# Optimization experiments

Hardware: AMD Instinct MI355X
Metric: run time of the kernel (lower is better)

## Reference

```python
import jax, jax.numpy as jnp
import numpy as np

STRIDE = 2
P = 2


def setup_inputs() -> dict:
    key = jax.random.key(0)
    x = jax.random.normal(key, (32, 256, 64, 64), dtype=jnp.float32)
    return {"x": x}


def reference(x) -> jnp.ndarray:
    s = STRIDE
    b, c, h, w = x.shape
    # circular pad on the right/bottom if spatial dims are odd
    pad_h = h % 2
    pad_w = w % 2
    if pad_h or pad_w:
        x = jnp.pad(x, ((0, 0), (0, 0), (0, pad_h), (0, pad_w)), mode="wrap")
    h2, w2 = x.shape[2] // s, x.shape[3] // s
    # all s*s polyphase components: comps[i*s+j] == x[:, :, i::s, j::s]
    comps = x.reshape(b, c, h2, s, w2, s)
    comps = comps.transpose(3, 5, 0, 1, 2, 4).reshape(s * s, b, c, h2, w2)
    # p-norm per (component, batch) over channels + spatial dims
    norms = jnp.sum(jnp.abs(comps) ** P, axis=(2, 3, 4)) ** (1.0 / P)  # [s*s, b]
    max_idx = jnp.argmax(norms, axis=0)  # [b]
    selected = comps[max_idx, jnp.arange(b)]  # [b, c, h2, w2]
    return selected
```

## Files before the change

kernel.cpp:

```cpp
#include <hip/hip_runtime.h>


#define B 32
#define C 256
#define H 64
#define W 64
#define H2 32
#define W2 32
#define NBLK 64
#define IN_F4_PER_BATCH (C * H * W / 4)
#define PAIRS_PER_BATCH (IN_F4_PER_BATCH / 2)
#define OUT_F4_PER_BATCH (C * H2 * W2 / 4)

typedef float floatx4 __attribute__((ext_vector_type(4)));

__global__ __launch_bounds__(256) void aps_partials(const float4* __restrict__ x,
                                                    float* __restrict__ ws) {
    const int b = blockIdx.y;
    const float4* xb = x + (size_t)b * IN_F4_PER_BATCH;
    float s0 = 0.f, s1 = 0.f, s2 = 0.f, s3 = 0.f;
    for (int g = blockIdx.x * blockDim.x + threadIdx.x; g < PAIRS_PER_BATCH;
         g += gridDim.x * blockDim.x) {
        const int base = ((g >> 4) << 5) + (g & 15);
        float4 ve = xb[base];
        float4 vo = xb[base + 16];
        s0 += ve.x * ve.x + ve.z * ve.z;
        s1 += ve.y * ve.y + ve.w * ve.w;
        s2 += vo.x * vo.x + vo.z * vo.z;
        s3 += vo.y * vo.y + vo.w * vo.w;
    }
    for (int off = 32; off; off >>= 1) {
        s0 += __shfl_down(s0, off);
        s1 += __shfl_down(s1, off);
        s2 += __shfl_down(s2, off);
        s3 += __shfl_down(s3, off);
    }
    __shared__ float sm[4][4];
    const int lane = threadIdx.x & 63;
    const int wave = threadIdx.x >> 6;
    if (lane == 0) {
        sm[wave][0] = s0; sm[wave][1] = s1; sm[wave][2] = s2; sm[wave][3] = s3;
    }
    __syncthreads();
    if (threadIdx.x < 4) {
        const int k = threadIdx.x;
        float t = sm[0][k] + sm[1][k] + sm[2][k] + sm[3][k];
        ws[(b * 4 + k) * NBLK + blockIdx.x] = t;
    }
}

__global__ __launch_bounds__(256) void aps_gather(const float* __restrict__ x,
                                                  const float* __restrict__ ws,
                                                  float* __restrict__ out) {
    const int b = blockIdx.y;
    const int lane = threadIdx.x & 63;
    const int wave = threadIdx.x >> 6;
    float p = ws[(b * 4 + wave) * NBLK + lane];
    for (int off = 32; off; off >>= 1) p += __shfl_down(p, off);
    __shared__ float s4[4];
    if (lane == 0) s4[wave] = p;
    __syncthreads();
    float v0 = s4[0], v1 = s4[1], v2 = s4[2], v3 = s4[3];
    float best = v0;
    int k = 0;
    if (v1 > best) { best = v1; k = 1; }
    if (v2 > best) { best = v2; k = 2; }
    if (v3 > best) { k = 3; }
    const int di = k >> 1;
    const int dj = k & 1;

    const int idx = blockIdx.x * blockDim.x + threadIdx.x;
    const int t4 = idx & 7;
    const int i  = (idx >> 3) & 31;
    const int c  = idx >> 8;
    const float* row = x + (((size_t)(b * C + c) * H) + (2 * i + di)) * W;
    const float4* r4 = (const float4*)row + 2 * t4;
    float4 a  = r4[0];
    float4 bb = r4[1];
    floatx4 o;
    if (dj == 0) { o.x = a.x; o.y = a.z; o.z = bb.x; o.w = bb.z; }
    else         { o.x = a.y; o.y = a.w; o.z = bb.y; o.w = bb.w; }
    floatx4* op = (floatx4*)(out + ((size_t)b * OUT_F4_PER_BATCH + idx) * 4);
    __builtin_nontemporal_store(o, op);
}

extern "C" void kernel_launch(void* const* d_in, const int* in_sizes, int n_in,
                              void* d_out, int out_size, void* d_ws, size_t ws_size,
                              hipStream_t stream) {
    const float* x = (const float*)d_in[0];
    float* out = (float*)d_out;
    float* ws = (float*)d_ws;

    aps_partials<<<dim3(NBLK, B), 256, 0, stream>>>((const float4*)x, ws);
    aps_gather<<<dim3(OUT_F4_PER_BATCH / 256, B), 256, 0, stream>>>(x, ws, out);
}
```

Measured before the change: 213.8 us.

## Restructure partial-norm and gather loops with fixed trip counts and float2 stores

The partial-sum kernel now reads contiguous float4s with a compile-time trip count and unroll. It keeps two accumulators and recovers the row parity from lane position through a partial shuffle reduction, instead of pairing even and odd rows per thread. The gather kernel uses fewer blocks that each loop over several elements, loading one float4 and storing a float2, rather than one thread per float4 output. Launch bounds add an occupancy hint. The aim is more memory-level parallelism and less index overhead, at the cost of narrower stores in the gather.

```diff
diff --git a/kernel.cpp b/kernel.cpp
--- a/kernel.cpp
+++ b/kernel.cpp
@@ -9,38 +9,37 @@
 #define W2 32
 #define NBLK 64
 #define IN_F4_PER_BATCH (C * H * W / 4)
-#define PAIRS_PER_BATCH (IN_F4_PER_BATCH / 2)
-#define OUT_F4_PER_BATCH (C * H2 * W2 / 4)
+#define T1 (NBLK * 256)
+#define ITER1 (IN_F4_PER_BATCH / T1)
+#define SEL_F2_PER_BATCH (C * H2 * W2 / 2)
+#define GBLK 128
+#define T2 (GBLK * 256)
+#define ITER2 (SEL_F2_PER_BATCH / T2)
 
-typedef float floatx4 __attribute__((ext_vector_type(4)));
+typedef float floatx2 __attribute__((ext_vector_type(2)));
 
-__global__ __launch_bounds__(256) void aps_partials(const float4* __restrict__ x,
-                                                    float* __restrict__ ws) {
+__global__ __launch_bounds__(256, 8) void aps_partials(const float4* __restrict__ x,
+                                                       float* __restrict__ ws) {
     const int b = blockIdx.y;
     const float4* xb = x + (size_t)b * IN_F4_PER_BATCH;
-    float s0 = 0.f, s1 = 0.f, s2 = 0.f, s3 = 0.f;
-    for (int g = blockIdx.x * blockDim.x + threadIdx.x; g < PAIRS_PER_BATCH;
-         g += gridDim.x * blockDim.x) {
-        const int base = ((g >> 4) << 5) + (g & 15);
-        float4 ve = xb[base];
-        float4 vo = xb[base + 16];
-        s0 += ve.x * ve.x + ve.z * ve.z;
-        s1 += ve.y * ve.y + ve.w * ve.w;
-        s2 += vo.x * vo.x + vo.z * vo.z;
-        s3 += vo.y * vo.y + vo.w * vo.w;
+    const int q0 = blockIdx.x * 256 + threadIdx.x;
+    float sA = 0.f, sB = 0.f;
+#pragma unroll 4
+    for (int it = 0; it < ITER1; ++it) {
+        float4 v = xb[q0 + it * T1];
+        sA += v.x * v.x + v.z * v.z;
+        sB += v.y * v.y + v.w * v.w;
     }
-    for (int off = 32; off; off >>= 1) {
-        s0 += __shfl_down(s0, off);
-        s1 += __shfl_down(s1, off);
-        s2 += __shfl_down(s2, off);
-        s3 += __shfl_down(s3, off);
+    sA += __shfl_down(sA, 32);  sB += __shfl_down(sB, 32);
+#pragma unroll
+    for (int off = 8; off; off >>= 1) {
+        sA += __shfl_down(sA, off);  sB += __shfl_down(sB, off);
     }
     __shared__ float sm[4][4];
     const int lane = threadIdx.x & 63;
     const int wave = threadIdx.x >> 6;
-    if (lane == 0) {
-        sm[wave][0] = s0; sm[wave][1] = s1; sm[wave][2] = s2; sm[wave][3] = s3;
-    }
+    if (lane == 0)  { sm[wave][0] = sA; sm[wave][1] = sB; }
+    if (lane == 16) { sm[wave][2] = sA; sm[wave][3] = sB; }
     __syncthreads();
     if (threadIdx.x < 4) {
         const int k = threadIdx.x;
@@ -49,9 +48,9 @@
     }
 }
 
-__global__ __launch_bounds__(256) void aps_gather(const float* __restrict__ x,
-                                                  const float* __restrict__ ws,
-                                                  float* __restrict__ out) {
+__global__ __launch_bounds__(256, 8) void aps_gather(const float4* __restrict__ x,
+                                                     const float* __restrict__ ws,
+                                                     floatx2* __restrict__ out) {
     const int b = blockIdx.y;
     const int lane = threadIdx.x & 63;
     const int wave = threadIdx.x >> 6;
@@ -60,7 +59,7 @@
     __shared__ float s4[4];
     if (lane == 0) s4[wave] = p;
     __syncthreads();
-    float v0 = s4[0], v1 = s4[1], v2 = s4[2], v3 = s4[3];
+    const float v0 = s4[0], v1 = s4[1], v2 = s4[2], v3 = s4[3];
     float best = v0;
     int k = 0;
     if (v1 > best) { best = v1; k = 1; }
@@ -69,19 +68,21 @@
     const int di = k >> 1;
     const int dj = k & 1;
 
-    const int idx = blockIdx.x * blockDim.x + threadIdx.x;
-    const int t4 = idx & 7;
-    const int i  = (idx >> 3) & 31;
-    const int c  = idx >> 8;
-    const float* row = x + (((size_t)(b * C + c) * H) + (2 * i + di)) * W;
-    const float4* r4 = (const float4*)row + 2 * t4;
-    float4 a  = r4[0];
-    float4 bb = r4[1];
-    floatx4 o;
-    if (dj == 0) { o.x = a.x; o.y = a.z; o.z = bb.x; o.w = bb.z; }
-    else         { o.x = a.y; o.y = a.w; o.z = bb.y; o.w = bb.w; }
-    floatx4* op = (floatx4*)(out + ((size_t)b * OUT_F4_PER_BATCH + idx) * 4);
-    __builtin_nontemporal_store(o, op);
+    const float4* xb = x + (size_t)b * IN_F4_PER_BATCH;
+    floatx2* ob = out + (size_t)b * SEL_F2_PER_BATCH;
+    const int m0 = blockIdx.x * 256 + threadIdx.x;
+#pragma unroll
+    for (int it = 0; it < ITER2; ++it) {
+        const int m   = m0 + it * T2;
+        const int ch  = m >> 9;
+        const int r   = (m >> 4) & 31;
+        const int col = m & 15;
+        float4 v = xb[(ch * 64 + 2 * r + di) * 16 + col];
+        floatx2 o;
+        if (dj == 0) { o.x = v.x; o.y = v.z; }
+        else         { o.x = v.y; o.y = v.w; }
+        __builtin_nontemporal_store(o, ob + m);
+    }
 }
 
 extern "C" void kernel_launch(void* const* d_in, const int* in_sizes, int n_in,
@@ -92,5 +93,5 @@
     float* ws = (float*)d_ws;
 
     aps_partials<<<dim3(NBLK, B), 256, 0, stream>>>((const float4*)x, ws);
-    aps_gather<<<dim3(OUT_F4_PER_BATCH / 256, B), 256, 0, stream>>>(x, ws, out);
+    aps_gather<<<dim3(GBLK, B), 256, 0, stream>>>((const float4*)x, ws, (floatx2*)out);
 }
```

After: 209.1 us. 2.2% less time.
